# Kernel optimization log

Hardware: AMD Instinct MI355X
Metric: run time of the kernel (lower is better)

## Reference

```python
import jax, jax.numpy as jnp
import numpy as np

B, S, DN, L = 2048, 8, 8, 50        # batch, n_sparse, n_dense, hist len
V, VF = 100000, 100000              # sparse vocab, feed vocab
ED, FD = 16, 512                    # sparse embed dim, feed embed dim
HID1, HID2 = 256, 128               # DNN hidden sizes
NE, NT, EO = 8, 4, 8                # experts, tasks, expert out dim
INPUT_DIM = ED * S + DN + FD + FD   # 1160


def setup_inputs() -> dict:
    key = jax.random.key(0)
    ks = jax.random.split(key, 20)
    sc = 0.02
    f32 = jnp.float32
    return {
        "sparse_ids": jax.random.randint(ks[0], (B, S), 0, V),
        "dense": jax.random.normal(ks[1], (B, DN), f32),
        "feedid": jax.random.randint(ks[2], (B,), 0, VF),
        "hist_feedid": jax.random.randint(ks[3], (B, L), 0, VF),
        "emb_tables": jax.random.normal(ks[4], (S, V, ED), f32) * sc,
        "feed_table": jax.random.normal(ks[5], (VF, FD), f32) * sc,
        "attn_w1": jax.random.normal(ks[6], (4 * FD, 128), f32) * sc,
        "attn_b1": jnp.zeros((128,), f32),
        "attn_w2": jax.random.normal(ks[7], (128, 1), f32) * sc,
        "attn_b2": jnp.zeros((1,), f32),
        "dnn_w1": jax.random.normal(ks[8], (INPUT_DIM, HID1), f32) * sc,
        "dnn_b1": jnp.zeros((HID1,), f32),
        "dnn_w2": jax.random.normal(ks[9], (HID1, HID2), f32) * sc,
        "dnn_b2": jnp.zeros((HID2,), f32),
        "expert_w": jax.random.normal(ks[10], (NE, HID2, EO), f32) * sc,
        "gate_w": jax.random.normal(ks[11], (NT, HID2, NE), f32) * sc,
        "out_w": jax.random.normal(ks[12], (NT, EO, 1), f32) * sc,
        "out_b": jnp.zeros((NT, 1), f32),
    }


def reference(sparse_ids, dense, feedid, hist_feedid,
              emb_tables, feed_table,
              attn_w1, attn_b1, attn_w2, attn_b2,
              dnn_w1, dnn_b1, dnn_w2, dnn_b2,
              expert_w, gate_w, out_w, out_b):
    # --- sparse embeddings: one table per feature -> [B, S, ED] -> flat ---
    embed = jax.vmap(lambda t, ids: t[ids], in_axes=(0, 1), out_axes=1)(
        emb_tables, sparse_ids)                       # [B, S, ED]
    sparse_flat = embed.reshape(embed.shape[0], -1)   # [B, S*ED]

    # --- feed / history embeddings ---
    feed = feed_table[feedid]                         # [B, FD]
    hist = feed_table[hist_feedid]                    # [B, L, FD]

    # --- DIN attention (query=feed, keys=hist) ---
    q = jnp.broadcast_to(feed[:, None, :], hist.shape)          # [B, L, FD]
    x = jnp.concatenate([q, hist, q - hist, q * hist], axis=-1)  # [B, L, 4FD]
    h = jax.nn.relu(x @ attn_w1 + attn_b1)                       # [B, L, 128]
    scores = (h @ attn_w2 + attn_b2)[..., 0]                     # [B, L]
    attn = jax.nn.softmax(scores, axis=1)
    user_interest = jnp.einsum('bl,bld->bd', attn, hist)         # [B, FD]

    # --- DNN (dropout off in eval) ---
    dnn_in = jnp.concatenate([sparse_flat, dense, feed, user_interest], axis=1)
    z = jax.nn.relu(dnn_in @ dnn_w1 + dnn_b1)
    dnn_out = jax.nn.relu(z @ dnn_w2 + dnn_b2)                   # [B, 128]

    # --- MMOE (eval: no expert dropout mask) ---
    expert_out = jnp.einsum('bi,eio->beo', dnn_out, expert_w)    # [B, NE, EO]
    gates = jax.nn.softmax(jnp.einsum('bi,tie->bte', dnn_out, gate_w), axis=-1)
    task_out = jnp.einsum('bte,beo->bto', gates, expert_out)     # [B, NT, EO]

    # --- per-task heads ---
    logits = jnp.einsum('bto,toh->bth', task_out, out_w) + out_b  # [B, NT, 1]
    return jax.nn.sigmoid(logits)
```

## Files before the change

kernel.cpp:

```cpp
#include <hip/hip_runtime.h>
#include <hip/hip_bf16.h>

typedef unsigned short u16;
typedef unsigned int u32;
typedef __attribute__((ext_vector_type(8))) short short8;
typedef __attribute__((ext_vector_type(8))) u16 ushort8;
typedef __attribute__((ext_vector_type(4))) float f32x4;

#define BB 2048
#define SS 8
#define DNUM 8
#define LL 50
#define EDIM 16
#define FDIM 512
#define HID1 256
#define HID2 128
#define VF 100000
#define KDNN 1216
#define ROWS (BB*LL)

__device__ inline u16 f2bf(float x) {
    return __builtin_bit_cast(u16, __float2bfloat16(x));
}
__device__ inline float bf2f(u16 b) {
    u32 u = ((u32)b) << 16;
    return __builtin_bit_cast(float, u);
}
__device__ inline void load16_lds(const void* g, void* l) {
    __builtin_amdgcn_global_load_lds(
        (const __attribute__((address_space(1))) u32*)g,
        (__attribute__((address_space(3))) u32*)l, 16, 0, 0);
}
__device__ inline float wave_sum(float v) {
    #pragma unroll
    for (int off = 32; off > 0; off >>= 1) v += __shfl_xor(v, off, 64);
    return v;
}
__device__ inline float wave_max(float v) {
    #pragma unroll
    for (int off = 32; off > 0; off >>= 1) v = fmaxf(v, __shfl_xor(v, off, 64));
    return v;
}
__device__ inline void cvt8(const float4& a, const float4& b, ushort8& o) {
    o[0]=f2bf(a.x); o[1]=f2bf(a.y); o[2]=f2bf(a.z); o[3]=f2bf(a.w);
    o[4]=f2bf(b.x); o[5]=f2bf(b.y); o[6]=f2bf(b.z); o[7]=f2bf(b.w);
}

#define PREP_BLKS 2112
__global__ __launch_bounds__(256) void prep_small(
    const float* __restrict__ ft,
    const float* __restrict__ w1, const float* __restrict__ dw1,
    const float* __restrict__ dw2,
    u16* __restrict__ WHP_T, u16* __restrict__ WQ_T,
    u16* __restrict__ W1D_T, u16* __restrict__ W2D_T,
    const int* __restrict__ sparse_ids, const float* __restrict__ dense,
    const int* __restrict__ feedid, const float* __restrict__ emb_tables,
    u16* __restrict__ dnn_in, u16* __restrict__ A_q)
{
    int blk = blockIdx.x, t = threadIdx.x;
    if (blk < PREP_BLKS) {
        int idx = blk * 256 + t;
        if (idx < 131072) {
            int n = idx >> 10, k = idx & 1023;
            float v;
            if (k < 512) v = w1[(512 + k) * 128 + n] - w1[(1024 + k) * 128 + n];
            else         v = w1[(1024 + k) * 128 + n];
            WHP_T[n * 1024 + k] = f2bf(v);
        } else if (idx < 196608) {
            int i = idx - 131072;
            int n = i >> 9, k = i & 511;
            WQ_T[n * 512 + k] = f2bf(w1[k * 128 + n] + w1[(1024 + k) * 128 + n]);
        } else if (idx < 507904) {
            int i = idx - 196608;
            int n = i / KDNN, k = i - n * KDNN;
            W1D_T[i] = (k < 1160) ? f2bf(dw1[k * HID1 + n]) : (u16)0;
        } else if (idx < 540672) {
            int i = idx - 507904;
            int n = i >> 8, k = i & 255;
            W2D_T[i] = f2bf(dw2[k * HID2 + n]);
        }
    } else {
        int b = blk - PREP_BLKS;
        u16* drow = dnn_in + (size_t)b * KDNN;
        if (t < 128) {
            int s = t >> 4, e = t & 15;
            int id = sparse_ids[b * SS + s];
            float v = emb_tables[(size_t)s * 1600000 + (size_t)id * EDIM + e];
            drow[t] = f2bf(v);
        } else if (t < 136) {
            drow[t] = f2bf(dense[b * DNUM + (t - 128)]);
        } else if (t < 192) {
            drow[1160 + (t - 136)] = 0;
        }
        int fid = feedid[b];
        float2 f = *(const float2*)&ft[(size_t)fid * FDIM + t * 2];
        u16 u0 = f2bf(f.x), u1 = f2bf(f.y);
        drow[136 + t * 2] = u0;
        drow[136 + t * 2 + 1] = u1;
        A_q[(size_t)b * FDIM + t * 2] = u0;
        A_q[(size_t)b * FDIM + t * 2 + 1] = u1;
    }
}

template<int BM, bool RELU, bool OUT_BF16>
__global__ __launch_bounds__(256, 4) void gemm_bt(
    const u16* __restrict__ A, int lda,
    const u16* __restrict__ BT, int ldb,
    const float* __restrict__ bias,
    void* __restrict__ Cv, int M, int N, int K)
{
    constexpr int MI = BM / 32;
    __shared__ u16 As[BM * 64];
    __shared__ u16 Bs[128 * 64];
    int m0 = blockIdx.x * BM, n0 = blockIdx.y * 128;
    int tid = threadIdx.x, wave = tid >> 6, lane = tid & 63;
    int lrow = lane >> 3, lk = (lane & 7) * 8;
    f32x4 acc[MI][4];
    f32x4 zz = {0.f, 0.f, 0.f, 0.f};
    #pragma unroll
    for (int i = 0; i < MI; i++)
        #pragma unroll
        for (int j = 0; j < 4; j++) acc[i][j] = zz;
    int wm = (wave >> 1) * (BM / 2), wn = (wave & 1) * 64;

    for (int kt = 0; kt < K; kt += 64) {
        #pragma unroll
        for (int j = 0; j < MI; ++j) {
            int c = wave * MI + j;
            int row = c * 8 + lrow;
            load16_lds(A + (size_t)(m0 + row) * lda + kt + lk, &As[c * 512]);
        }
        #pragma unroll
        for (int j = 0; j < 4; ++j) {
            int c = wave * 4 + j;
            int row = c * 8 + lrow;
            load16_lds(BT + (size_t)(n0 + row) * ldb + kt + lk, &Bs[c * 512]);
        }
        __syncthreads();
        #pragma unroll
        for (int ks = 0; ks < 2; ++ks) {
            int kk = ks * 32 + (lane >> 4) * 8;
            short8 af[MI], bf[4];
            #pragma unroll
            for (int i = 0; i < MI; i++)
                af[i] = *(const short8*)&As[(wm + i * 16 + (lane & 15)) * 64 + kk];
            #pragma unroll
            for (int j = 0; j < 4; j++)
                bf[j] = *(const short8*)&Bs[(wn + j * 16 + (lane & 15)) * 64 + kk];
            #pragma unroll
            for (int i = 0; i < MI; i++)
                #pragma unroll
                for (int j = 0; j < 4; j++)
                    acc[i][j] = __builtin_amdgcn_mfma_f32_16x16x32_bf16(
                        af[i], bf[j], acc[i][j], 0, 0, 0);
        }
        __syncthreads();
    }
    #pragma unroll
    for (int i = 0; i < MI; i++) {
        #pragma unroll
        for (int j = 0; j < 4; j++) {
            #pragma unroll
            for (int r = 0; r < 4; r++) {
                int row = m0 + wm + i * 16 + (lane >> 4) * 4 + r;
                int col = n0 + wn + j * 16 + (lane & 15);
                float v = acc[i][j][r];
                if (bias) v += bias[col];
                if (RELU) v = fmaxf(v, 0.f);
                size_t off = (size_t)row * N + col;
                if (OUT_BF16) ((u16*)Cv)[off] = f2bf(v);
                else ((float*)Cv)[off] = v;
            }
        }
    }
}

#define MFMA_BF16 __builtin_amdgcn_mfma_f32_16x16x32_bf16

__global__ __launch_bounds__(256, 4) void din_gemm(
    const int* __restrict__ hist_ids, const int* __restrict__ feedid,
    const float* __restrict__ ft, const u16* __restrict__ WHP_T,
    const float* __restrict__ qw, const float* __restrict__ b1,
    const float* __restrict__ w2v, float* __restrict__ scores)
{
    __shared__ float Asf[2][64 * 32];
    __shared__ u16 BsH[128 * 32];
    __shared__ u16 BsP[128 * 32];
    __shared__ u16 qls[3 * 512];
    __shared__ float qbs[3 * 128];
    __shared__ float w2s[128];
    __shared__ float sred[64 * 2];

    int t = threadIdx.x, w = t >> 6, lane = t & 63;
    int m0 = blockIdx.x * 64, b0 = m0 / LL;
    int fr = lane & 15, kg8 = (lane >> 4) * 8;
    int wm = (w >> 1) * 32, wn = (w & 1) * 64;

    for (int idx = t; idx < 384; idx += 256) {
        int bi = idx >> 7, col = idx & 127;
        int bb = b0 + bi; if (bb > BB - 1) bb = BB - 1;
        qbs[idx] = qw[bb * 128 + col] + b1[col];
    }
    if (t < 128) w2s[t] = w2v[t];
    for (int idx = t; idx < 768; idx += 256) {
        int bi = idx >> 8, d2 = (idx & 255) * 2;
        int bb = b0 + bi; if (bb > BB - 1) bb = BB - 1;
        float2 qv = *(const float2*)&ft[(size_t)feedid[bb] * FDIM + d2];
        qls[bi * 512 + d2] = f2bf(qv.x);
        qls[bi * 512 + d2 + 1] = f2bf(qv.y);
    }

    const float* a_src0 = ft + (size_t)hist_ids[m0 + w * 16 + fr] * FDIM
                             + (lane >> 4) * 4;
    const float* a_src1 = a_src0 + 16;
    const u16* b_src0 = WHP_T + (size_t)(w * 32 + (lane >> 2)) * 1024 + (lane & 3) * 8;
    const u16* b_src1 = b_src0 + 16 * 1024;

    int qb0 = (m0 + wm + fr) / LL - b0;
    int qb1 = (m0 + wm + 16 + fr) / LL - b0;

    f32x4 acc[2][4];
    f32x4 zz = {0.f, 0.f, 0.f, 0.f};
    #pragma unroll
    for (int i = 0; i < 2; i++)
        #pragma unroll
        for (int j = 0; j < 4; j++) acc[i][j] = zz;

    load16_lds(a_src0,        &Asf[0][w * 512]);
    load16_lds(a_src1,        &Asf[0][w * 512 + 256]);
    load16_lds(b_src0,        &BsH[(w * 2) * 512]);
    load16_lds(b_src1,        &BsH[(w * 2 + 1) * 512]);
    load16_lds(b_src0 + 512,  &BsP[(w * 2) * 512]);
    load16_lds(b_src1 + 512,  &BsP[(w * 2 + 1) * 512]);
    load16_lds(a_src0 + 32,   &Asf[1][w * 512]);
    load16_lds(a_src1 + 32,   &Asf[1][w * 512 + 256]);
    asm volatile("s_waitcnt vmcnt(2) lgkmcnt(0)" ::: "memory");
    __builtin_amdgcn_s_barrier();

    int ws0 = wm >> 4;
    int k4a = (lane >> 4) * 2;
    int offA0 = ws0 * 512 + k4a * 64 + fr * 4;
    int offA1 = (ws0 + 1) * 512 + k4a * 64 + fr * 4;

    #pragma unroll
    for (int kt = 0; kt < 16; ++kt) {
        const int buf = kt & 1;
        const int ko = kt * 32;
        float4 h0a = *(const float4*)&Asf[buf][offA0];
        float4 h0b = *(const float4*)&Asf[buf][offA0 + 64];
        float4 h1a = *(const float4*)&Asf[buf][offA1];
        float4 h1b = *(const float4*)&Asf[buf][offA1 + 64];
        ushort8 hv0, hv1;
        cvt8(h0a, h0b, hv0);
        cvt8(h1a, h1b, hv1);
        ushort8 qv0 = *(const ushort8*)&qls[qb0 * 512 + ko + kg8];
        ushort8 qv1 = *(const ushort8*)&qls[qb1 * 512 + ko + kg8];
        short8 bh[4], bp[4];
        #pragma unroll
        for (int j = 0; j < 4; ++j) {
            int n = wn + j * 16 + fr;
            bh[j] = *(const short8*)&BsH[n * 32 + kg8];
            bp[j] = *(const short8*)&BsP[n * 32 + kg8];
        }
        short8 ah0 = __builtin_bit_cast(short8, hv0);
        short8 ah1 = __builtin_bit_cast(short8, hv1);
        #pragma unroll
        for (int j = 0; j < 4; ++j) {
            acc[0][j] = MFMA_BF16(ah0, bh[j], acc[0][j], 0, 0, 0);
            acc[1][j] = MFMA_BF16(ah1, bh[j], acc[1][j], 0, 0, 0);
        }
        ushort8 pv0, pv1;
        #pragma unroll
        for (int e = 0; e < 8; ++e) {
            pv0[e] = f2bf(bf2f(hv0[e]) * bf2f(qv0[e]));
            pv1[e] = f2bf(bf2f(hv1[e]) * bf2f(qv1[e]));
        }
        short8 ap0 = __builtin_bit_cast(short8, pv0);
        short8 ap1 = __builtin_bit_cast(short8, pv1);
        #pragma unroll
        for (int j = 0; j < 4; ++j) {
            acc[0][j] = MFMA_BF16(ap0, bp[j], acc[0][j], 0, 0, 0);
            acc[1][j] = MFMA_BF16(ap1, bp[j], acc[1][j], 0, 0, 0);
        }
        asm volatile("s_waitcnt lgkmcnt(0)" ::: "memory");
        __builtin_amdgcn_s_barrier();
        if (kt < 15) {
            const int knB = (kt + 1) * 32;
            load16_lds(b_src0 + knB,       &BsH[(w * 2) * 512]);
            load16_lds(b_src1 + knB,       &BsH[(w * 2 + 1) * 512]);
            load16_lds(b_src0 + 512 + knB, &BsP[(w * 2) * 512]);
            load16_lds(b_src1 + 512 + knB, &BsP[(w * 2 + 1) * 512]);
            if (kt < 14) {
                const int knA = (kt + 2) * 32;
                load16_lds(a_src0 + knA, &Asf[buf][w * 512]);
                load16_lds(a_src1 + knA, &Asf[buf][w * 512 + 256]);
                asm volatile("s_waitcnt vmcnt(2)" ::: "memory");
            } else {
                asm volatile("s_waitcnt vmcnt(0)" ::: "memory");
            }
            __builtin_amdgcn_s_barrier();
        }
    }

    #pragma unroll
    for (int i = 0; i < 2; ++i) {
        #pragma unroll
        for (int r = 0; r < 4; ++r) {
            int rl = wm + i * 16 + (lane >> 4) * 4 + r;
            int bi = (m0 + rl) / LL - b0;
            float s = 0.f;
            #pragma unroll
            for (int j = 0; j < 4; ++j) {
                int col = wn + j * 16 + fr;
                float v = acc[i][j][r] + qbs[bi * 128 + col];
                s += fmaxf(v, 0.f) * w2s[col];
            }
            s += __shfl_xor(s, 1, 64);
            s += __shfl_xor(s, 2, 64);
            s += __shfl_xor(s, 4, 64);
            s += __shfl_xor(s, 8, 64);
            if (fr == 0) sred[rl * 2 + (w & 1)] = s;
        }
    }
    __syncthreads();
    if (t < 64) scores[m0 + t] = sred[t * 2] + sred[t * 2 + 1];
}

__global__ __launch_bounds__(256) void softmax_ui(
    const float* __restrict__ scores, const int* __restrict__ hist_ids,
    const float* __restrict__ feed_table, u16* __restrict__ dnn_in)
{
    int b = blockIdx.x, t = threadIdx.x;
    int wave = t >> 6, lane = t & 63;
    __shared__ float sc[56];
    __shared__ int hid[56];
    if (t >= 64 && t < 64 + LL) hid[t - 64] = hist_ids[b * LL + (t - 64)];
    if (wave == 0) {
        float x = (lane < LL) ? scores[b * LL + lane] : -1e30f;
        float mx = wave_max(x);
        float e = (lane < LL) ? __expf(x - mx) : 0.f;
        float s = wave_sum(e);
        if (lane < LL) sc[lane] = e / s;
    }
    __syncthreads();
    int d = t * 2;
    float a0 = 0.f, a1 = 0.f;
    #pragma unroll 5
    for (int l = 0; l < LL; ++l) {
        float2 hv = *(const float2*)&feed_table[(size_t)hid[l] * FDIM + d];
        float al = sc[l];
        a0 += al * hv.x;
        a1 += al * hv.y;
    }
    dnn_in[(size_t)b * KDNN + 648 + d] = f2bf(a0);
    dnn_in[(size_t)b * KDNN + 648 + d + 1] = f2bf(a1);
}

__global__ __launch_bounds__(256) void mmoe_head(
    const float* __restrict__ dnn_out, const float* __restrict__ expert_w,
    const float* __restrict__ gate_w, const float* __restrict__ out_w,
    const float* __restrict__ out_b, float* __restrict__ out)
{
    int wave = threadIdx.x >> 6, lane = threadIdx.x & 63;
    int b = blockIdx.x * 4 + wave;
    __shared__ float ds[4][128];
    __shared__ float eo[4][64];
    __shared__ float gt[4][32];
    ds[wave][lane] = dnn_out[b * 128 + lane];
    ds[wave][lane + 64] = dnn_out[b * 128 + 64 + lane];
    __syncthreads();
    int e = lane >> 3, o = lane & 7;
    float acc = 0.f;
    for (int k = 0; k < 128; ++k)
        acc += ds[wave][k] * expert_w[(e * 128 + k) * 8 + o];
    eo[wave][lane] = acc;
    if (lane < 32) {
        int tt = lane >> 3, ee = lane & 7;
        float g = 0.f;
        for (int k = 0; k < 128; ++k)
            g += ds[wave][k] * gate_w[(tt * 128 + k) * 8 + ee];
        float m = g;
        #pragma unroll
        for (int off = 4; off; off >>= 1) m = fmaxf(m, __shfl_xor(m, off, 8));
        float ex = __expf(g - m);
        float s = ex;
        #pragma unroll
        for (int off = 4; off; off >>= 1) s += __shfl_xor(s, off, 8);
        gt[wave][lane] = ex / s;
    }
    __syncthreads();
    if (lane < 32) {
        int tt = lane >> 3, o2 = lane & 7;
        float to = 0.f;
        #pragma unroll
        for (int ee = 0; ee < 8; ++ee)
            to += gt[wave][tt * 8 + ee] * eo[wave][ee * 8 + o2];
        float pl = to * out_w[tt * 8 + o2];
        #pragma unroll
        for (int off = 4; off; off >>= 1) pl += __shfl_xor(pl, off, 8);
        if (o2 == 0) {
            float logit = pl + out_b[tt];
            out[b * 4 + tt] = 1.f / (1.f + __expf(-logit));
        }
    }
}

extern "C" void kernel_launch(void* const* d_in, const int* in_sizes, int n_in,
                              void* d_out, int out_size, void* d_ws, size_t ws_size,
                              hipStream_t stream)
{
    const int*   sparse_ids = (const int*)d_in[0];
    const float* dense      = (const float*)d_in[1];
    const int*   feedid     = (const int*)d_in[2];
    const int*   hist_ids   = (const int*)d_in[3];
    const float* emb_tables = (const float*)d_in[4];
    const float* feed_table = (const float*)d_in[5];
    const float* attn_w1    = (const float*)d_in[6];
    const float* attn_b1    = (const float*)d_in[7];
    const float* attn_w2    = (const float*)d_in[8];
    const float* attn_b2    = (const float*)d_in[9];
    const float* dnn_w1     = (const float*)d_in[10];
    const float* dnn_b1     = (const float*)d_in[11];
    const float* dnn_w2     = (const float*)d_in[12];
    const float* dnn_b2     = (const float*)d_in[13];
    const float* expert_w   = (const float*)d_in[14];
    const float* gate_w     = (const float*)d_in[15];
    const float* out_w      = (const float*)d_in[16];
    const float* out_b      = (const float*)d_in[17];
    float* out = (float*)d_out;
    (void)attn_b2;

    char* ws = (char*)d_ws;
    size_t off = 0;
    auto alloc = [&](size_t bytes) {
        char* p = ws + off;
        off += (bytes + 255) & ~(size_t)255;
        return p;
    };
    u16* WHP_T = (u16*)alloc(131072 * 2);
    u16* WQ_T  = (u16*)alloc(65536 * 2);
    u16* W1D_T = (u16*)alloc((size_t)HID1 * KDNN * 2);
    u16* W2D_T = (u16*)alloc((size_t)HID2 * HID1 * 2);
    u16* AQ    = (u16*)alloc((size_t)BB * FDIM * 2);
    float* QW  = (float*)alloc((size_t)BB * 128 * 4);
    u16* DNNIN = (u16*)alloc((size_t)BB * KDNN * 2);
    u16* Z     = (u16*)alloc((size_t)BB * HID1 * 2);
    float* DOUT= (float*)alloc((size_t)BB * HID2 * 4);
    float* SCORES = (float*)alloc((size_t)ROWS * 4);

    prep_small<<<PREP_BLKS + BB, 256, 0, stream>>>(
        feed_table, attn_w1, dnn_w1, dnn_w2,
        WHP_T, WQ_T, W1D_T, W2D_T,
        sparse_ids, dense, feedid, emb_tables, DNNIN, AQ);
    gemm_bt<32, false, false><<<dim3(BB / 32, 1), 256, 0, stream>>>(
        AQ, 512, WQ_T, 512, nullptr, QW, BB, 128, 512);
    din_gemm<<<ROWS / 64, 256, 0, stream>>>(
        hist_ids, feedid, feed_table, WHP_T, QW, attn_b1, attn_w2, SCORES);
    softmax_ui<<<BB, 256, 0, stream>>>(SCORES, hist_ids, feed_table, DNNIN);
    gemm_bt<32, true, true><<<dim3(BB / 32, HID1 / 128), 256, 0, stream>>>(
        DNNIN, KDNN, W1D_T, KDNN, dnn_b1, Z, BB, HID1, KDNN);
    gemm_bt<32, true, false><<<dim3(BB / 32, 1), 256, 0, stream>>>(
        Z, HID1, W2D_T, HID1, dnn_b2, DOUT, BB, HID2, HID1);
    mmoe_head<<<BB / 4, 256, 0, stream>>>(DOUT, expert_w, gate_w, out_w,
                                          out_b, out);
}
```

Before: 150.2 us.

## Fuse DIN attention GEMM with softmax and weighted history sum per batch row

Replaces the row-tiled attention-score GEMM and the separate softmax/weighted-sum kernel with one kernel that handles one batch element per block. Scores stay in shared memory, softmax and the user-interest reduction run in the same block, and the query vector and bias become single per-block vectors. This removes a launch and the scores round trip through global memory. In exchange each block pads 50 history rows to a 64-row tile, adding wasted MFMA work and more weight-tile loads.

After: 138.7 us. 1.08x faster.

```diff
diff --git a/kernel.cpp b/kernel.cpp
--- a/kernel.cpp
+++ b/kernel.cpp
@@ -177,47 +177,45 @@
 
 #define MFMA_BF16 __builtin_amdgcn_mfma_f32_16x16x32_bf16
 
-__global__ __launch_bounds__(256, 4) void din_gemm(
+__global__ __launch_bounds__(256, 4) void din_fused(
     const int* __restrict__ hist_ids, const int* __restrict__ feedid,
     const float* __restrict__ ft, const u16* __restrict__ WHP_T,
     const float* __restrict__ qw, const float* __restrict__ b1,
-    const float* __restrict__ w2v, float* __restrict__ scores)
+    const float* __restrict__ w2v, u16* __restrict__ dnn_in)
 {
     __shared__ float Asf[2][64 * 32];
     __shared__ u16 BsH[128 * 32];
     __shared__ u16 BsP[128 * 32];
-    __shared__ u16 qls[3 * 512];
-    __shared__ float qbs[3 * 128];
+    __shared__ u16 qls[512];
+    __shared__ float qbs[128];
     __shared__ float w2s[128];
     __shared__ float sred[64 * 2];
-
+    __shared__ float scf[64];
+    __shared__ int hids[64];
+
+    int b = blockIdx.x;
     int t = threadIdx.x, w = t >> 6, lane = t & 63;
-    int m0 = blockIdx.x * 64, b0 = m0 / LL;
     int fr = lane & 15, kg8 = (lane >> 4) * 8;
     int wm = (w >> 1) * 32, wn = (w & 1) * 64;
-
-    for (int idx = t; idx < 384; idx += 256) {
-        int bi = idx >> 7, col = idx & 127;
-        int bb = b0 + bi; if (bb > BB - 1) bb = BB - 1;
-        qbs[idx] = qw[bb * 128 + col] + b1[col];
-    }
-    if (t < 128) w2s[t] = w2v[t];
-    for (int idx = t; idx < 768; idx += 256) {
-        int bi = idx >> 8, d2 = (idx & 255) * 2;
-        int bb = b0 + bi; if (bb > BB - 1) bb = BB - 1;
-        float2 qv = *(const float2*)&ft[(size_t)feedid[bb] * FDIM + d2];
-        qls[bi * 512 + d2] = f2bf(qv.x);
-        qls[bi * 512 + d2 + 1] = f2bf(qv.y);
-    }
-
-    const float* a_src0 = ft + (size_t)hist_ids[m0 + w * 16 + fr] * FDIM
+    int fid = feedid[b];
+
+    if (t < 64) hids[t] = hist_ids[b * LL + (t < LL ? t : LL - 1)];
+    if (t < 128) {
+        qbs[t] = qw[b * 128 + t] + b1[t];
+        w2s[t] = w2v[t];
+    }
+    {
+        float2 qv = *(const float2*)&ft[(size_t)fid * FDIM + t * 2];
+        qls[t * 2] = f2bf(qv.x);
+        qls[t * 2 + 1] = f2bf(qv.y);
+    }
+
+    int srow = w * 16 + fr;
+    const float* a_src0 = ft + (size_t)hist_ids[b * LL + (srow < LL ? srow : LL - 1)] * FDIM
                              + (lane >> 4) * 4;
     const float* a_src1 = a_src0 + 16;
     const u16* b_src0 = WHP_T + (size_t)(w * 32 + (lane >> 2)) * 1024 + (lane & 3) * 8;
     const u16* b_src1 = b_src0 + 16 * 1024;
-
-    int qb0 = (m0 + wm + fr) / LL - b0;
-    int qb1 = (m0 + wm + 16 + fr) / LL - b0;
 
     f32x4 acc[2][4];
     f32x4 zz = {0.f, 0.f, 0.f, 0.f};
@@ -253,8 +251,7 @@
         ushort8 hv0, hv1;
         cvt8(h0a, h0b, hv0);
         cvt8(h1a, h1b, hv1);
-        ushort8 qv0 = *(const ushort8*)&qls[qb0 * 512 + ko + kg8];
-        ushort8 qv1 = *(const ushort8*)&qls[qb1 * 512 + ko + kg8];
+        ushort8 qv = *(const ushort8*)&qls[ko + kg8];
         short8 bh[4], bp[4];
         #pragma unroll
         for (int j = 0; j < 4; ++j) {
@@ -272,8 +269,8 @@
         ushort8 pv0, pv1;
         #pragma unroll
         for (int e = 0; e < 8; ++e) {
-            pv0[e] = f2bf(bf2f(hv0[e]) * bf2f(qv0[e]));
-            pv1[e] = f2bf(bf2f(hv1[e]) * bf2f(qv1[e]));
+            pv0[e] = f2bf(bf2f(hv0[e]) * bf2f(qv[e]));
+            pv1[e] = f2bf(bf2f(hv1[e]) * bf2f(qv[e]));
         }
         short8 ap0 = __builtin_bit_cast(short8, pv0);
         short8 ap1 = __builtin_bit_cast(short8, pv1);
@@ -307,12 +304,11 @@
         #pragma unroll
         for (int r = 0; r < 4; ++r) {
             int rl = wm + i * 16 + (lane >> 4) * 4 + r;
-            int bi = (m0 + rl) / LL - b0;
             float s = 0.f;
             #pragma unroll
             for (int j = 0; j < 4; ++j) {
                 int col = wn + j * 16 + fr;
-                float v = acc[i][j][r] + qbs[bi * 128 + col];
+                float v = acc[i][j][r] + qbs[col];
                 s += fmaxf(v, 0.f) * w2s[col];
             }
             s += __shfl_xor(s, 1, 64);
@@ -323,32 +319,22 @@
         }
     }
     __syncthreads();
-    if (t < 64) scores[m0 + t] = sred[t * 2] + sred[t * 2 + 1];
-}
-
-__global__ __launch_bounds__(256) void softmax_ui(
-    const float* __restrict__ scores, const int* __restrict__ hist_ids,
-    const float* __restrict__ feed_table, u16* __restrict__ dnn_in)
-{
-    int b = blockIdx.x, t = threadIdx.x;
-    int wave = t >> 6, lane = t & 63;
-    __shared__ float sc[56];
-    __shared__ int hid[56];
-    if (t >= 64 && t < 64 + LL) hid[t - 64] = hist_ids[b * LL + (t - 64)];
-    if (wave == 0) {
-        float x = (lane < LL) ? scores[b * LL + lane] : -1e30f;
+    if (t < 64) scf[t] = sred[t * 2] + sred[t * 2 + 1];
+    __syncthreads();
+    if (w == 0) {
+        float x = (lane < LL) ? scf[lane] : -1e30f;
         float mx = wave_max(x);
         float e = (lane < LL) ? __expf(x - mx) : 0.f;
         float s = wave_sum(e);
-        if (lane < LL) sc[lane] = e / s;
+        scf[lane] = (lane < LL) ? e / s : 0.f;
     }
     __syncthreads();
     int d = t * 2;
     float a0 = 0.f, a1 = 0.f;
     #pragma unroll 5
     for (int l = 0; l < LL; ++l) {
-        float2 hv = *(const float2*)&feed_table[(size_t)hid[l] * FDIM + d];
-        float al = sc[l];
+        float2 hv = *(const float2*)&ft[(size_t)hids[l] * FDIM + d];
+        float al = scf[l];
         a0 += al * hv.x;
         a1 += al * hv.y;
     }
@@ -446,7 +432,6 @@
     u16* DNNIN = (u16*)alloc((size_t)BB * KDNN * 2);
     u16* Z     = (u16*)alloc((size_t)BB * HID1 * 2);
     float* DOUT= (float*)alloc((size_t)BB * HID2 * 4);
-    float* SCORES = (float*)alloc((size_t)ROWS * 4);
 
     prep_small<<<PREP_BLKS + BB, 256, 0, stream>>>(
         feed_table, attn_w1, dnn_w1, dnn_w2,
@@ -454,9 +439,8 @@
         sparse_ids, dense, feedid, emb_tables, DNNIN, AQ);
     gemm_bt<32, false, false><<<dim3(BB / 32, 1), 256, 0, stream>>>(
         AQ, 512, WQ_T, 512, nullptr, QW, BB, 128, 512);
-    din_gemm<<<ROWS / 64, 256, 0, stream>>>(
-        hist_ids, feedid, feed_table, WHP_T, QW, attn_b1, attn_w2, SCORES);
-    softmax_ui<<<BB, 256, 0, stream>>>(SCORES, hist_ids, feed_table, DNNIN);
+    din_fused<<<BB, 256, 0, stream>>>(
+        hist_ids, feedid, feed_table, WHP_T, QW, attn_b1, attn_w2, DNNIN);
     gemm_bt<32, true, true><<<dim3(BB / 32, HID1 / 128), 256, 0, stream>>>(
         DNNIN, KDNN, W1D_T, KDNN, dnn_b1, Z, BB, HID1, KDNN);
     gemm_bt<32, true, false><<<dim3(BB / 32, 1), 256, 0, stream>>>(
```
